# Optimization experiments

Measured on AMD Instinct MI355X. Metric: run time of the kernel, lower is better.

Reference implementation:

```python
import jax, jax.numpy as jnp
import numpy as np

NEG_INF = -1.0e9


def setup_inputs() -> dict:
    key = jax.random.key(0)
    ks = jax.random.split(key, 8)
    B, H, S, D = 8, 8, 1024, 64
    return {
        "gv_feat": jax.random.normal(ks[0], (B, D), dtype=jnp.float32),
        "query2": jax.random.normal(ks[1], (B, H, S, D), dtype=jnp.float32),
        "key": jax.random.normal(ks[2], (B, H, S, D), dtype=jnp.float32),
        "att_mask": jax.random.randint(ks[3], (B, S), 0, 2, dtype=jnp.int32),
        "value1": jax.random.normal(ks[4], (B, H, S, D), dtype=jnp.float32),
        "value2": jax.random.normal(ks[5], (B, H, S, D), dtype=jnp.float32),
        "W_ch": jax.random.normal(ks[6], (D, D), dtype=jnp.float32) * (1.0 / np.sqrt(D)),
        "b_ch": jnp.zeros((D,), dtype=jnp.float32),
    }


def reference(gv_feat, query2, key, att_mask, value1, value2, W_ch, b_ch):
    # query2/key/value1/value2: [B, H, S, D]; att_mask: [B, S]
    D = query2.shape[-1]
    scaling = D ** (-0.5)
    # spatial attention: masked scaled QK^T softmax
    scores = jnp.einsum("bhqd,bhkd->bhqk", query2, key) * scaling  # [B,H,S,S]
    mask = att_mask[:, None, None, :]  # [B,1,1,S]
    scores = jnp.where(mask == 0, NEG_INF, scores)
    alpha_spatial = jax.nn.softmax(scores, axis=-1)
    attn2 = jnp.einsum("bhqk,bhkd->bhqd", alpha_spatial, value2)  # [B,H,S,D]
    # channel attention: sigmoid-gated linear over elementwise value1*key
    att_map_channel = value1 * key  # [B,H,S,D]
    alpha_channel = jax.nn.sigmoid(
        jnp.einsum("bhsd,ed->bhse", att_map_channel, W_ch) + b_ch
    )
    attn2 = alpha_channel * attn2
    return (gv_feat, attn2)
```

## Files before the change

### kernel.cpp

```cpp
#include <hip/hip_runtime.h>
#include <hip/hip_bf16.h>

typedef __attribute__((ext_vector_type(4)))  float f32x4;
typedef __attribute__((ext_vector_type(16))) float f32x16;
typedef __attribute__((ext_vector_type(8)))  short bf16x8;
typedef __attribute__((ext_vector_type(4)))  unsigned u32x4;
typedef __attribute__((ext_vector_type(2)))  unsigned u32x2;

#define NEG_INF_F (-1000000000.0f)

__device__ inline unsigned pkbf(float a, float b) {
    union { __hip_bfloat16 h; unsigned short u; } x, y;
    x.h = __float2bfloat16(a);
    y.h = __float2bfloat16(b);
    return (unsigned)x.u | ((unsigned)y.u << 16);
}

__global__ __launch_bounds__(1024) void aoa_prep_kernel(
    const int* __restrict__ maskp,
    int* __restrict__ vidx, float* __restrict__ padmask, int* __restrict__ nvalid)
{
    const int b   = blockIdx.x;
    const int tid = threadIdx.x;
    const int lane = tid & 63;

    const int m = maskp[b * 1024 + tid] ? 1 : 0;
    unsigned long long bal = __ballot(m);
    const int wpre = __popcll(bal & ((1ull << lane) - 1ull));

    __shared__ int wsum[16], woff[16];
    if (lane == 63) wsum[tid >> 6] = wpre + m;
    __syncthreads();
    if (tid < 16) {
        int off = 0;
        for (int i = 0; i < tid; ++i) off += wsum[i];
        woff[tid] = off;
    }
    __syncthreads();
    const int pos = woff[tid >> 6] + wpre;
    const int nv  = woff[15] + wsum[15];

    if (m) vidx[b * 1024 + pos] = tid;
    if (tid >= nv) vidx[b * 1024 + tid] = 0;
    padmask[b * 1024 + tid] = (tid < nv) ? 0.0f : NEG_INF_F;
    if (tid == 0) nvalid[b] = nv;
}

__global__ __launch_bounds__(512) void aoa_attn_kernel(
    const float* __restrict__ gv,
    const float* __restrict__ q2,
    const float* __restrict__ keyp,
    const float* __restrict__ v1,
    const float* __restrict__ v2,
    const float* __restrict__ W,
    const float* __restrict__ bch,
    const int*   __restrict__ vidx,
    const float* __restrict__ padmask,
    const int*   __restrict__ nvalid,
    float* __restrict__ out)
{
    constexpr int S = 1024, D = 64;
    const int bh  = blockIdx.x;
    const int qt  = blockIdx.y;
    const int b   = bh >> 3;
    const int tid = threadIdx.x;
    const int wid = tid >> 6;
    const int lane = tid & 63;
    const int l31 = lane & 31;
    const int h   = lane >> 5;

    float* out_attn = out + 512;
    if (bh == 0 && qt == 0) out[tid] = gv[tid];

    __shared__ float pmL[S];
    __shared__ int   vidxL[S];
    __shared__ short Klds[2][64][72];
    __shared__ short Vt[2][64][72];
    __shared__ float Lw[8][32];

    for (int i = tid; i < S; i += 512) {
        pmL[i]   = padmask[b * S + i];
        vidxL[i] = vidx[b * S + i];
    }

    const int nv = nvalid[b];
    const int NT = (nv + 63) >> 6;

    const size_t base = (size_t)bh * S * D;
    const float* Qp  = q2   + base;
    const float* Kp  = keyp + base;
    const float* V1p = v1   + base;
    const float* V2p = v2   + base;

    const int q0   = qt * 256 + wid * 32;
    const int qrow = q0 + l31;

    bf16x8 bq[4];
    #pragma unroll
    for (int ds = 0; ds < 4; ++ds) {
        const f32x4* p = (const f32x4*)(Qp + (size_t)qrow * D + ds * 16 + h * 8);
        f32x4 x0 = p[0], x1 = p[1];
        u32x4 u = (u32x4){pkbf(x0[0], x0[1]), pkbf(x0[2], x0[3]),
                          pkbf(x1[0], x1[1]), pkbf(x1[2], x1[3])};
        bq[ds] = *(bf16x8*)&u;
    }

    f32x16 acc_o[2];
    #pragma unroll
    for (int dh = 0; dh < 2; ++dh)
        #pragma unroll
        for (int r = 0; r < 16; ++r) acc_o[dh][r] = 0.0f;

    float m_run = -1e30f, l_run = 0.0f;
    const float SC = 0.125f * 1.4426950408889634f;

    const int kk   = tid >> 3;
    const int d0   = (tid & 7) << 3;
    const int dcol = tid & 63;
    const int kr0  = (tid >> 6) << 3;

    __syncthreads();

    f32x4 kA, kB;
    float vv[8];
    {
        const f32x4* src = (const f32x4*)(Kp + (size_t)vidxL[kk] * D + d0);
        kA = src[0]; kB = src[1];
        #pragma unroll
        for (int i = 0; i < 8; ++i) vv[i] = V2p[(size_t)vidxL[kr0 + i] * D + dcol];
    }
    *(u32x4*)&Klds[0][kk][d0] = (u32x4){pkbf(kA[0], kA[1]), pkbf(kA[2], kA[3]),
                                        pkbf(kB[0], kB[1]), pkbf(kB[2], kB[3])};
    *(u32x4*)&Vt[0][dcol][kr0] = (u32x4){pkbf(vv[0], vv[1]), pkbf(vv[2], vv[3]),
                                         pkbf(vv[4], vv[5]), pkbf(vv[6], vv[7])};
    int cur = 0;

    for (int t = 0; t < NT; ++t) {
        const int kt = t * 64;
        __syncthreads();

        if (t < NT - 1) {
            const f32x4* src = (const f32x4*)(Kp + (size_t)vidxL[kt + 64 + kk] * D + d0);
            kA = src[0]; kB = src[1];
            #pragma unroll
            for (int i = 0; i < 8; ++i) vv[i] = V2p[(size_t)vidxL[kt + 64 + kr0 + i] * D + dcol];
        }

        f32x16 a0;
        #pragma unroll
        for (int r = 0; r < 16; ++r) a0[r] = 0.0f;
        #pragma unroll
        for (int ds = 0; ds < 4; ++ds) {
            bf16x8 ak = *(const bf16x8*)&Klds[cur][l31][ds * 16 + h * 8];
            a0 = __builtin_amdgcn_mfma_f32_32x32x16_bf16(ak, bq[ds], a0, 0, 0, 0);
        }
        f32x16 a1;
        #pragma unroll
        for (int r = 0; r < 16; ++r) a1[r] = 0.0f;
        #pragma unroll
        for (int ds = 0; ds < 4; ++ds) {
            bf16x8 ak = *(const bf16x8*)&Klds[cur][32 + l31][ds * 16 + h * 8];
            a1 = __builtin_amdgcn_mfma_f32_32x32x16_bf16(ak, bq[ds], a1, 0, 0, 0);
        }

        unsigned w0[8];
        {
            float s[16], tmax = -1e30f;
            #pragma unroll
            for (int g = 0; g < 4; ++g) {
                f32x4 mk = *(const f32x4*)&pmL[kt + g * 8 + h * 4];
                #pragma unroll
                for (int j = 0; j < 4; ++j) {
                    float val = fmaf(a0[g * 4 + j], SC, mk[j]);
                    s[g * 4 + j] = val;
                    tmax = fmaxf(tmax, val);
                }
            }
            tmax = fmaxf(tmax, __shfl_xor(tmax, 32));
            if (__any(tmax > m_run + 8.0f)) {
                float mnew = fmaxf(m_run, tmax);
                float r = __builtin_amdgcn_exp2f(m_run - mnew);
                l_run *= r;
                #pragma unroll
                for (int dh = 0; dh < 2; ++dh)
                    #pragma unroll
                    for (int r2 = 0; r2 < 16; ++r2) acc_o[dh][r2] *= r;
                m_run = mnew;
            }
            float ps0 = 0.f, ps1 = 0.f;
            #pragma unroll
            for (int i = 0; i < 8; ++i) {
                float p0 = __builtin_amdgcn_exp2f(s[2 * i]     - m_run);
                float p1 = __builtin_amdgcn_exp2f(s[2 * i + 1] - m_run);
                ps0 += p0; ps1 += p1;
                w0[i] = pkbf(p0, p1);
            }
            float psum = ps0 + ps1;
            psum += __shfl_xor(psum, 32);
            l_run += psum;
        }

        #pragma unroll
        for (int t2 = 0; t2 < 2; ++t2) {
            u32x2 r0 = __builtin_amdgcn_permlane32_swap(w0[t2 * 4 + 0], w0[t2 * 4 + 2], false, false);
            u32x2 r1 = __builtin_amdgcn_permlane32_swap(w0[t2 * 4 + 1], w0[t2 * 4 + 3], false, false);
            u32x4 ua = (u32x4){r0[0], r1[0], r0[1], r1[1]};
            bf16x8 pa = *(bf16x8*)&ua;
            #pragma unroll
            for (int dh = 0; dh < 2; ++dh) {
                bf16x8 bv = *(const bf16x8*)&Vt[cur][dh * 32 + l31][t2 * 16 + h * 8];
                acc_o[dh] = __builtin_amdgcn_mfma_f32_32x32x16_bf16(pa, bv, acc_o[dh], 0, 0, 0);
            }
        }

        unsigned w1[8];
        {
            float s[16], tmax = -1e30f;
            #pragma unroll
            for (int g = 0; g < 4; ++g) {
                f32x4 mk = *(const f32x4*)&pmL[kt + 32 + g * 8 + h * 4];
                #pragma unroll
                for (int j = 0; j < 4; ++j) {
                    float val = fmaf(a1[g * 4 + j], SC, mk[j]);
                    s[g * 4 + j] = val;
                    tmax = fmaxf(tmax, val);
                }
            }
            tmax = fmaxf(tmax, __shfl_xor(tmax, 32));
            if (__any(tmax > m_run + 8.0f)) {
                float mnew = fmaxf(m_run, tmax);
                float r = __builtin_amdgcn_exp2f(m_run - mnew);
                l_run *= r;
                #pragma unroll
                for (int dh = 0; dh < 2; ++dh)
                    #pragma unroll
                    for (int r2 = 0; r2 < 16; ++r2) acc_o[dh][r2] *= r;
                m_run = mnew;
            }
            float ps0 = 0.f, ps1 = 0.f;
            #pragma unroll
            for (int i = 0; i < 8; ++i) {
                float p0 = __builtin_amdgcn_exp2f(s[2 * i]     - m_run);
                float p1 = __builtin_amdgcn_exp2f(s[2 * i + 1] - m_run);
                ps0 += p0; ps1 += p1;
                w1[i] = pkbf(p0, p1);
            }
            float psum = ps0 + ps1;
            psum += __shfl_xor(psum, 32);
            l_run += psum;
        }

        #pragma unroll
        for (int t2 = 0; t2 < 2; ++t2) {
            u32x2 r0 = __builtin_amdgcn_permlane32_swap(w1[t2 * 4 + 0], w1[t2 * 4 + 2], false, false);
            u32x2 r1 = __builtin_amdgcn_permlane32_swap(w1[t2 * 4 + 1], w1[t2 * 4 + 3], false, false);
            u32x4 ua = (u32x4){r0[0], r1[0], r0[1], r1[1]};
            bf16x8 pa = *(bf16x8*)&ua;
            #pragma unroll
            for (int dh = 0; dh < 2; ++dh) {
                bf16x8 bv = *(const bf16x8*)&Vt[cur][dh * 32 + l31][32 + t2 * 16 + h * 8];
                acc_o[dh] = __builtin_amdgcn_mfma_f32_32x32x16_bf16(pa, bv, acc_o[dh], 0, 0, 0);
            }
        }

        if (t < NT - 1) {
            *(u32x4*)&Klds[cur ^ 1][kk][d0] = (u32x4){pkbf(kA[0], kA[1]), pkbf(kA[2], kA[3]),
                                                      pkbf(kB[0], kB[1]), pkbf(kB[2], kB[3])};
            *(u32x4*)&Vt[cur ^ 1][dcol][kr0] = (u32x4){pkbf(vv[0], vv[1]), pkbf(vv[2], vv[3]),
                                                       pkbf(vv[4], vv[5]), pkbf(vv[6], vv[7])};
        }
        cur ^= 1;
    }

    f32x16 acc_g[2];
    #pragma unroll
    for (int eh = 0; eh < 2; ++eh)
        #pragma unroll
        for (int r = 0; r < 16; ++r) acc_g[eh][r] = 0.0f;

    bf16x8 bam[4];
    #pragma unroll
    for (int ds = 0; ds < 4; ++ds) {
        const f32x4* p1 = (const f32x4*)(V1p + (size_t)qrow * D + ds * 16 + h * 8);
        const f32x4* pk = (const f32x4*)(Kp  + (size_t)qrow * D + ds * 16 + h * 8);
        f32x4 a0 = p1[0], a1 = p1[1], c0 = pk[0], c1 = pk[1];
        u32x4 u = (u32x4){pkbf(a0[0]*c0[0], a0[1]*c0[1]), pkbf(a0[2]*c0[2], a0[3]*c0[3]),
                          pkbf(a1[0]*c1[0], a1[1]*c1[1]), pkbf(a1[2]*c1[2], a1[3]*c1[3])};
        bam[ds] = *(bf16x8*)&u;
    }
    #pragma unroll
    for (int eh = 0; eh < 2; ++eh) {
        #pragma unroll
        for (int ds = 0; ds < 4; ++ds) {
            const f32x4* pw = (const f32x4*)(W + (size_t)(eh * 32 + l31) * D + ds * 16 + h * 8);
            f32x4 x0 = pw[0], x1 = pw[1];
            u32x4 u = (u32x4){pkbf(x0[0], x0[1]), pkbf(x0[2], x0[3]),
                              pkbf(x1[0], x1[1]), pkbf(x1[2], x1[3])};
            bf16x8 bw = *(bf16x8*)&u;
            acc_g[eh] = __builtin_amdgcn_mfma_f32_32x32x16_bf16(bam[ds], bw, acc_g[eh], 0, 0, 0);
        }
    }

    Lw[wid][l31] = 1.0f / l_run;
    __builtin_amdgcn_wave_barrier();
    const float bv0 = bch[l31], bv1 = bch[32 + l31];
    #pragma unroll
    for (int dh = 0; dh < 2; ++dh) {
        const float bc = dh ? bv1 : bv0;
        #pragma unroll
        for (int r = 0; r < 16; ++r) {
            const int ql = (r & 3) + 8 * (r >> 2) + 4 * h;
            float invl = Lw[wid][ql];
            float o = acc_o[dh][r] * invl;
            float z = acc_g[dh][r] + bc;
            float gate = 1.0f / (1.0f + __expf(-z));
            out_attn[base + (size_t)(q0 + ql) * D + dh * 32 + l31] = o * gate;
        }
    }
}

extern "C" void kernel_launch(void* const* d_in, const int* in_sizes, int n_in,
                              void* d_out, int out_size, void* d_ws, size_t ws_size,
                              hipStream_t stream) {
    const float* gv   = (const float*)d_in[0];
    const float* q2   = (const float*)d_in[1];
    const float* keyp = (const float*)d_in[2];
    const int*   mask = (const int*)  d_in[3];
    const float* v1   = (const float*)d_in[4];
    const float* v2   = (const float*)d_in[5];
    const float* W    = (const float*)d_in[6];
    const float* bch  = (const float*)d_in[7];
    float* out = (float*)d_out;

    int*   vidx    = (int*)d_ws;
    float* padmask = (float*)(vidx + 8 * 1024);
    int*   nvalid  = (int*)(padmask + 8 * 1024);

    aoa_prep_kernel<<<8, 1024, 0, stream>>>(mask, vidx, padmask, nvalid);

    dim3 grid(64, 4);
    aoa_attn_kernel<<<grid, 512, 0, stream>>>(gv, q2, keyp, v1, v2, W, bch,
                                              vidx, padmask, nvalid, out);
}
```

Before: 41.36 us.

## Pre-gather and pre-convert K/V to compacted bf16 buffers in separate kernel

Adds a gather kernel that compacts the unmasked key and value2 rows into bf16 workspace buffers, with V stored transposed. The attention kernel then streams contiguous bf16 tiles instead of doing indexed fp32 gathers and conversions per tile. Before, each of the four query-tile blocks per head repeated this gather and conversion. The cost is an extra launch plus a round trip through global memory for the compacted K/V.

```diff
diff --git a/kernel.cpp b/kernel.cpp
--- a/kernel.cpp
+++ b/kernel.cpp
@@ -46,15 +46,61 @@
     if (tid == 0) nvalid[b] = nv;
 }
 
+__global__ __launch_bounds__(256) void aoa_gather_kernel(
+    const float* __restrict__ keyp, const float* __restrict__ v2,
+    const int* __restrict__ vidx,
+    short* __restrict__ Kc, short* __restrict__ Vtc)
+{
+    const int bh  = blockIdx.x;
+    const int c   = blockIdx.y;
+    const int tid = threadIdx.x;
+    const int b   = bh >> 3;
+    const size_t base = (size_t)bh * 65536;
+
+    __shared__ short T[64][72];
+
+    const int k    = tid >> 2;
+    const int dseg = (tid & 3) << 4;
+    const int pos  = c * 64 + k;
+    const int idx  = vidx[b * 1024 + pos];
+
+    {
+        const f32x4* ks = (const f32x4*)(keyp + base + (size_t)idx * 64 + dseg);
+        f32x4 a0 = ks[0], a1 = ks[1], a2 = ks[2], a3 = ks[3];
+        u32x4 w0 = (u32x4){pkbf(a0[0],a0[1]), pkbf(a0[2],a0[3]), pkbf(a1[0],a1[1]), pkbf(a1[2],a1[3])};
+        u32x4 w1 = (u32x4){pkbf(a2[0],a2[1]), pkbf(a2[2],a2[3]), pkbf(a3[0],a3[1]), pkbf(a3[2],a3[3])};
+        short* kd = Kc + base + (size_t)pos * 64 + dseg;
+        *(u32x4*)kd = w0; *(u32x4*)(kd + 8) = w1;
+
+        const f32x4* vs = (const f32x4*)(v2 + base + (size_t)idx * 64 + dseg);
+        f32x4 b0 = vs[0], b1 = vs[1], b2 = vs[2], b3 = vs[3];
+        u32x4 t0 = (u32x4){pkbf(b0[0],b0[1]), pkbf(b0[2],b0[3]), pkbf(b1[0],b1[1]), pkbf(b1[2],b1[3])};
+        u32x4 t1 = (u32x4){pkbf(b2[0],b2[1]), pkbf(b2[2],b2[3]), pkbf(b3[0],b3[1]), pkbf(b3[2],b3[3])};
+        *(u32x4*)&T[k][dseg]     = t0;
+        *(u32x4*)&T[k][dseg + 8] = t1;
+    }
+    __syncthreads();
+    {
+        const int d    = tid >> 2;
+        const int kseg = (tid & 3) << 4;
+        short tmp[16];
+        #pragma unroll
+        for (int i = 0; i < 16; ++i) tmp[i] = T[kseg + i][d];
+        short* vd = Vtc + base + (size_t)d * 1024 + c * 64 + kseg;
+        *(u32x4*)vd       = *(u32x4*)&tmp[0];
+        *(u32x4*)(vd + 8) = *(u32x4*)&tmp[8];
+    }
+}
+
 __global__ __launch_bounds__(512) void aoa_attn_kernel(
     const float* __restrict__ gv,
     const float* __restrict__ q2,
     const float* __restrict__ keyp,
     const float* __restrict__ v1,
-    const float* __restrict__ v2,
     const float* __restrict__ W,
     const float* __restrict__ bch,
-    const int*   __restrict__ vidx,
+    const short* __restrict__ Kc,
+    const short* __restrict__ Vtc,
     const float* __restrict__ padmask,
     const int*   __restrict__ nvalid,
     float* __restrict__ out)
@@ -73,15 +119,12 @@
     if (bh == 0 && qt == 0) out[tid] = gv[tid];
 
     __shared__ float pmL[S];
-    __shared__ int   vidxL[S];
     __shared__ short Klds[2][64][72];
     __shared__ short Vt[2][64][72];
     __shared__ float Lw[8][32];
 
-    for (int i = tid; i < S; i += 512) {
-        pmL[i]   = padmask[b * S + i];
-        vidxL[i] = vidx[b * S + i];
-    }
+    for (int i = tid; i < S; i += 512)
+        pmL[i] = padmask[b * S + i];
 
     const int nv = nvalid[b];
     const int NT = (nv + 63) >> 6;
@@ -90,7 +133,8 @@
     const float* Qp  = q2   + base;
     const float* Kp  = keyp + base;
     const float* V1p = v1   + base;
-    const float* V2p = v2   + base;
+    const short* Kcb = Kc  + base;
+    const short* Vcb = Vtc + base;
 
     const int q0   = qt * 256 + wid * 32;
     const int qrow = q0 + l31;
@@ -116,23 +160,13 @@
 
     const int kk   = tid >> 3;
     const int d0   = (tid & 7) << 3;
-    const int dcol = tid & 63;
-    const int kr0  = (tid >> 6) << 3;
-
-    __syncthreads();
-
-    f32x4 kA, kB;
-    float vv[8];
-    {
-        const f32x4* src = (const f32x4*)(Kp + (size_t)vidxL[kk] * D + d0);
-        kA = src[0]; kB = src[1];
-        #pragma unroll
-        for (int i = 0; i < 8; ++i) vv[i] = V2p[(size_t)vidxL[kr0 + i] * D + dcol];
-    }
-    *(u32x4*)&Klds[0][kk][d0] = (u32x4){pkbf(kA[0], kA[1]), pkbf(kA[2], kA[3]),
-                                        pkbf(kB[0], kB[1]), pkbf(kB[2], kB[3])};
-    *(u32x4*)&Vt[0][dcol][kr0] = (u32x4){pkbf(vv[0], vv[1]), pkbf(vv[2], vv[3]),
-                                         pkbf(vv[4], vv[5]), pkbf(vv[6], vv[7])};
+    const int vd   = tid & 63;
+    const int vk0  = (tid >> 6) << 3;
+
+    u32x4 kw = *(const u32x4*)(Kcb + (size_t)kk * 64 + d0);
+    u32x4 vw = *(const u32x4*)(Vcb + (size_t)vd * 1024 + vk0);
+    *(u32x4*)&Klds[0][kk][d0] = kw;
+    *(u32x4*)&Vt[0][vd][vk0]  = vw;
     int cur = 0;
 
     for (int t = 0; t < NT; ++t) {
@@ -140,10 +174,8 @@
         __syncthreads();
 
         if (t < NT - 1) {
-            const f32x4* src = (const f32x4*)(Kp + (size_t)vidxL[kt + 64 + kk] * D + d0);
-            kA = src[0]; kB = src[1];
-            #pragma unroll
-            for (int i = 0; i < 8; ++i) vv[i] = V2p[(size_t)vidxL[kt + 64 + kr0 + i] * D + dcol];
+            kw = *(const u32x4*)(Kcb + (size_t)(kt + 64 + kk) * 64 + d0);
+            vw = *(const u32x4*)(Vcb + (size_t)vd * 1024 + kt + 64 + vk0);
         }
 
         f32x16 a0;
@@ -264,10 +296,8 @@
         }
 
         if (t < NT - 1) {
-            *(u32x4*)&Klds[cur ^ 1][kk][d0] = (u32x4){pkbf(kA[0], kA[1]), pkbf(kA[2], kA[3]),
-                                                      pkbf(kB[0], kB[1]), pkbf(kB[2], kB[3])};
-            *(u32x4*)&Vt[cur ^ 1][dcol][kr0] = (u32x4){pkbf(vv[0], vv[1]), pkbf(vv[2], vv[3]),
-                                                       pkbf(vv[4], vv[5]), pkbf(vv[6], vv[7])};
+            *(u32x4*)&Klds[cur ^ 1][kk][d0] = kw;
+            *(u32x4*)&Vt[cur ^ 1][vd][vk0]  = vw;
         }
         cur ^= 1;
     }
@@ -332,13 +362,18 @@
     const float* bch  = (const float*)d_in[7];
     float* out = (float*)d_out;
 
-    int*   vidx    = (int*)d_ws;
+    short* Kc      = (short*)d_ws;
+    short* Vtc     = Kc + 64ull * 1024 * 64;
+    int*   vidx    = (int*)(Vtc + 64ull * 1024 * 64);
     float* padmask = (float*)(vidx + 8 * 1024);
     int*   nvalid  = (int*)(padmask + 8 * 1024);
 
     aoa_prep_kernel<<<8, 1024, 0, stream>>>(mask, vidx, padmask, nvalid);
 
+    dim3 ggrid(64, 16);
+    aoa_gather_kernel<<<ggrid, 256, 0, stream>>>(keyp, v2, vidx, Kc, Vtc);
+
     dim3 grid(64, 4);
-    aoa_attn_kernel<<<grid, 512, 0, stream>>>(gv, q2, keyp, v1, v2, W, bch,
-                                              vidx, padmask, nvalid, out);
-}
+    aoa_attn_kernel<<<grid, 512, 0, stream>>>(gv, q2, keyp, v1, W, bch,
+                                              Kc, Vtc, padmask, nvalid, out);
+}
```

Result: slower. 46.24 us (+11.8%).
